# Kernel optimization log

Measured on AMD Instinct MI355X. Metric: run time of the kernel, lower is better.

## Reference

```python
import jax, jax.numpy as jnp
import numpy as np

EMBED_DIM = 1024
NUM_HEADS = 16
HEAD_DIM = EMBED_DIM // NUM_HEADS


def setup_inputs() -> dict:
    key = jax.random.key(0)
    ks = jax.random.split(key, 9)
    B, L, D = 4, 2048, EMBED_DIM
    s = 1.0 / np.sqrt(D)
    return {
        "inputs": jax.random.normal(ks[0], (B, L, D), dtype=jnp.float32),
        "wq": jax.random.normal(ks[1], (D, D), dtype=jnp.float32) * s,
        "bq": jax.random.normal(ks[2], (D,), dtype=jnp.float32) * s,
        "wk": jax.random.normal(ks[3], (D, D), dtype=jnp.float32) * s,
        "bk": jax.random.normal(ks[4], (D,), dtype=jnp.float32) * s,
        "wv": jax.random.normal(ks[5], (D, D), dtype=jnp.float32) * s,
        "bv": jax.random.normal(ks[6], (D,), dtype=jnp.float32) * s,
        "wo": jax.random.normal(ks[7], (D, D), dtype=jnp.float32) * s,
        "bo": jax.random.normal(ks[8], (D,), dtype=jnp.float32) * s,
    }


def reference(inputs, wq, bq, wk, bk, wv, bv, wo, bo):
    B, L, D = inputs.shape
    H, Hd = NUM_HEADS, HEAD_DIM
    # Linear projections (torch Linear: x @ W^T + b)
    q = inputs @ wq.T + bq
    k = inputs @ wk.T + bk
    v = inputs @ wv.T + bv
    # (B, L, D) -> (B, H, L, Hd)
    q = q.reshape(B, L, H, Hd).transpose(0, 2, 1, 3)
    k = k.reshape(B, L, H, Hd).transpose(0, 2, 1, 3)
    v = v.reshape(B, L, H, Hd).transpose(0, 2, 1, 3)
    scale = 1.0 / np.sqrt(Hd).astype(np.float32)
    scores = jnp.einsum("bhqd,bhkd->bhqk", q, k) * scale  # (B,H,L,L)
    attn = jax.nn.softmax(scores, axis=-1)
    out = jnp.einsum("bhqk,bhkd->bhqd", attn, v)  # (B,H,L,Hd)
    out = out.transpose(0, 2, 1, 3).reshape(B, L, D)
    return out @ wo.T + bo
```

## Files before the change

kernel.cpp:

```cpp
#include <hip/hip_runtime.h>

typedef __attribute__((ext_vector_type(8))) short short8;
typedef __attribute__((ext_vector_type(8))) unsigned short ushort8;
typedef __attribute__((ext_vector_type(4))) unsigned short ushort4_t;
typedef __attribute__((ext_vector_type(4))) unsigned u32x4;
typedef __attribute__((ext_vector_type(4))) float f32x4;
typedef __attribute__((ext_vector_type(16))) float f32x16;

#define GLOAD_LDS(gp, lp) \
  __builtin_amdgcn_global_load_lds((const __attribute__((address_space(1))) void*)(gp), \
                                   (__attribute__((address_space(3))) void*)(lp), 16, 0, 0)

static __device__ __forceinline__ unsigned short f2bf(float f) {
  unsigned int u = __float_as_uint(f);
  u = u + 0x7fffu + ((u >> 16) & 1u);
  return (unsigned short)(u >> 16);
}

static __device__ __forceinline__ float exp2i(float x) {
  float r;
  asm("v_exp_f32 %0, %1" : "=v"(r) : "v"(x));
  return r;
}

static __device__ __forceinline__ unsigned cvtpk(float a, float b) {
  unsigned r;
  asm("v_cvt_pk_bf16_f32 %0, %1, %2" : "=v"(r) : "v"(a), "v"(b));
  return r;
}

static __device__ __forceinline__ void pl32swap(unsigned& a, unsigned& b) {
  asm("v_permlane32_swap_b32 %0, %1" : "+v"(a), "+v"(b));
}

__global__ __launch_bounds__(256) void cvt_bf16(const float* __restrict__ in,
                                                unsigned short* __restrict__ out,
                                                int n) {
  int i = (blockIdx.x * 256 + threadIdx.x) * 8;
  if (i >= n) return;
  const float4* p = reinterpret_cast<const float4*>(in + i);
  float4 a = p[0], b = p[1];
  ushort8 o;
  o[0] = f2bf(a.x); o[1] = f2bf(a.y); o[2] = f2bf(a.z); o[3] = f2bf(a.w);
  o[4] = f2bf(b.x); o[5] = f2bf(b.y); o[6] = f2bf(b.z); o[7] = f2bf(b.w);
  *reinterpret_cast<ushort8*>(out + i) = o;
}

__global__ __launch_bounds__(256) void cvt_w4(const float* __restrict__ i0, const float* __restrict__ i1,
                                              const float* __restrict__ i2, const float* __restrict__ i3,
                                              unsigned short* __restrict__ o0, unsigned short* __restrict__ o1,
                                              unsigned short* __restrict__ o2, unsigned short* __restrict__ o3) {
  int w = blockIdx.y;
  const float* in = (w == 0) ? i0 : (w == 1) ? i1 : (w == 2) ? i2 : i3;
  unsigned short* out = (w == 0) ? o0 : (w == 1) ? o1 : (w == 2) ? o2 : o3;
  int i = (blockIdx.x * 256 + threadIdx.x) * 8;
  const float4* p = reinterpret_cast<const float4*>(in + i);
  float4 a = p[0], b = p[1];
  ushort8 o;
  o[0] = f2bf(a.x); o[1] = f2bf(a.y); o[2] = f2bf(a.z); o[3] = f2bf(a.w);
  o[4] = f2bf(b.x); o[5] = f2bf(b.y); o[6] = f2bf(b.z); o[7] = f2bf(b.w);
  *reinterpret_cast<ushort8*>(out + i) = o;
}

template <int MODE>
__global__ __launch_bounds__(256) void gemm_bt(const unsigned short* __restrict__ A,
                                               const unsigned short* __restrict__ B,
                                               const float* __restrict__ bias,
                                               void* __restrict__ Cptr,
                                               int M, int N, int K, float scale) {
  __shared__ char As[2][16384];
  __shared__ char Bs[2][16384];
  const int t = threadIdx.x;
  const int lane = t & 63, wave = t >> 6;
  const int wm = wave >> 1, wn = wave & 1;
  const int m0 = blockIdx.y * 128, n0 = blockIdx.x * 128;

  const unsigned short* aS[4];
  const unsigned short* bS[4];
#pragma unroll
  for (int j = 0; j < 4; j++) {
    int i = wave * 256 + j * 64 + lane;
    int r = i >> 3, c = ((i & 7) ^ (r & 7)) << 3;
    aS[j] = A + (size_t)(m0 + r) * K + c;
    bS[j] = B + (size_t)(n0 + r) * K + c;
  }

  f32x4 acc[4][4] = {};
  const int NT = K >> 6;

#pragma unroll
  for (int j = 0; j < 4; j++) {
    GLOAD_LDS(aS[j], As[0] + wave * 4096 + j * 1024);
    GLOAD_LDS(bS[j], Bs[0] + wave * 4096 + j * 1024);
  }

  for (int kt = 0; kt < NT; kt++) {
    const int cur = kt & 1;
    __syncthreads();
    if (kt + 1 < NT) {
      int ko = (kt + 1) << 6;
#pragma unroll
      for (int j = 0; j < 4; j++) {
        GLOAD_LDS(aS[j] + ko, As[cur ^ 1] + wave * 4096 + j * 1024);
        GLOAD_LDS(bS[j] + ko, Bs[cur ^ 1] + wave * 4096 + j * 1024);
      }
    }
    const char* Ac = As[cur];
    const char* Bc = Bs[cur];
#pragma unroll
    for (int ks = 0; ks < 2; ks++) {
      short8 af[4], bfr[4];
#pragma unroll
      for (int x = 0; x < 4; x++) {
        int arow = wm * 64 + x * 16 + (lane & 15);
        int kk = ks * 32 + (lane >> 4) * 8;
        af[x] = *reinterpret_cast<const short8*>(Ac + (((arow * 64 + kk) * 2) ^ ((arow & 7) << 4)));
        int brow = wn * 64 + x * 16 + (lane & 15);
        bfr[x] = *reinterpret_cast<const short8*>(Bc + (((brow * 64 + kk) * 2) ^ ((brow & 7) << 4)));
      }
      __builtin_amdgcn_s_setprio(1);
#pragma unroll
      for (int mi = 0; mi < 4; mi++)
#pragma unroll
        for (int ni = 0; ni < 4; ni++)
          acc[mi][ni] = __builtin_amdgcn_mfma_f32_16x16x32_bf16(af[mi], bfr[ni], acc[mi][ni], 0, 0, 0);
      __builtin_amdgcn_s_setprio(0);
    }
  }

#pragma unroll
  for (int mi = 0; mi < 4; mi++) {
#pragma unroll
    for (int ni = 0; ni < 4; ni++) {
      int n = n0 + wn * 64 + ni * 16 + (lane & 15);
      float bs = bias[n];
      int mbase = m0 + wm * 64 + mi * 16 + ((lane >> 4) << 2);
      if (MODE == 2) {
        int b = mbase >> 11, l = mbase & 2047;
        ushort4_t o;
#pragma unroll
        for (int r = 0; r < 4; r++) o[r] = f2bf(acc[mi][ni][r] + bs);
        *reinterpret_cast<ushort4_t*>((unsigned short*)Cptr + (size_t)(b * N + n) * 2048 + l) = o;
      } else if (MODE == 0) {
#pragma unroll
        for (int r = 0; r < 4; r++)
          ((unsigned short*)Cptr)[(size_t)(mbase + r) * N + n] = f2bf((acc[mi][ni][r] + bs) * scale);
      } else {
#pragma unroll
        for (int r = 0; r < 4; r++)
          ((float*)Cptr)[(size_t)(mbase + r) * N + n] = acc[mi][ni][r] + bs;
      }
    }
  }
}

__global__ __launch_bounds__(256) void attn_fwd(const unsigned short* __restrict__ Q,
                                                const unsigned short* __restrict__ Kb,
                                                const unsigned short* __restrict__ Vt,
                                                unsigned short* __restrict__ O) {
  const int h = blockIdx.y;
  const int b = blockIdx.z;
  const int q0 = blockIdx.x * 128;
  __shared__ char Ks[2][8192];
  __shared__ char Vs[2][8192];
  const int t = threadIdx.x, lane = t & 63, wave = t >> 6;
  const int ql = lane & 31;
  const int hi = lane >> 5;
  const int qrow = q0 + wave * 32 + ql;
  const int sw = (ql & 7) << 4;

  int lo_[4];
#pragma unroll
  for (int st = 0; st < 4; st++) lo_[st] = (ql * 128 + sw) ^ (st * 32 + hi * 16);

  const int ic0 = wave * 128 + lane, ic1 = ic0 + 64;
  const int r0 = ic0 >> 3, c0 = ((ic0 & 7) ^ (r0 & 7)) << 3;
  const int r1 = ic1 >> 3, c1 = ((ic1 & 7) ^ (r1 & 7)) << 3;
  const unsigned short* kS0 = Kb + (size_t)(b * 2048 + r0) * 1024 + h * 64 + c0;
  const unsigned short* kS1 = Kb + (size_t)(b * 2048 + r1) * 1024 + h * 64 + c1;
  const unsigned short* vS0 = Vt + ((size_t)(b * 16 + h) * 64 + r0) * 2048 + c0;
  const unsigned short* vS1 = Vt + ((size_t)(b * 16 + h) * 64 + r1) * 2048 + c1;

  short8 qf[4];
  {
    const unsigned short* qp = Q + (size_t)(b * 2048 + qrow) * 1024 + h * 64 + hi * 8;
#pragma unroll
    for (int st = 0; st < 4; st++) qf[st] = *reinterpret_cast<const short8*>(qp + st * 16);
  }

  const short one_bf = (short)0x3F80;
  const short8 ones = {one_bf, one_bf, one_bf, one_bf, one_bf, one_bf, one_bf, one_bf};

  f32x16 accd0 = {}, accd1 = {};
  f32x16 accl = {};

  GLOAD_LDS(kS0, Ks[0] + wave * 2048);
  GLOAD_LDS(kS1, Ks[0] + wave * 2048 + 1024);
  GLOAD_LDS(vS0, Vs[0] + wave * 2048);
  GLOAD_LDS(vS1, Vs[0] + wave * 2048 + 1024);

#pragma unroll 2
  for (int kt = 0; kt < 32; kt++) {
    const int cur = kt & 1;
    __syncthreads();
    if (kt + 1 < 32) {
      size_t ko = (size_t)(kt + 1) * 65536;
      int vo = (kt + 1) * 64;
      GLOAD_LDS(kS0 + ko, Ks[cur ^ 1] + wave * 2048);
      GLOAD_LDS(kS1 + ko, Ks[cur ^ 1] + wave * 2048 + 1024);
      GLOAD_LDS(vS0 + vo, Vs[cur ^ 1] + wave * 2048);
      GLOAD_LDS(vS1 + vo, Vs[cur ^ 1] + wave * 2048 + 1024);
    }
    const char* Kc = Ks[cur];
    const char* Vc = Vs[cur];

    f32x16 s0 = {}, s1 = {};
    __builtin_amdgcn_s_setprio(1);
#pragma unroll
    for (int st = 0; st < 4; st++) {
      short8 k0 = *reinterpret_cast<const short8*>(Kc + lo_[st]);
      short8 k1 = *reinterpret_cast<const short8*>(Kc + lo_[st] + 4096);
      s0 = __builtin_amdgcn_mfma_f32_32x32x16_bf16(k0, qf[st], s0, 0, 0, 0);
      s1 = __builtin_amdgcn_mfma_f32_32x32x16_bf16(k1, qf[st], s1, 0, 0, 0);
    }
    __builtin_amdgcn_s_setprio(0);

#pragma unroll
    for (int r = 0; r < 16; r++) s0[r] = exp2i(s0[r]);
#pragma unroll
    for (int r = 0; r < 16; r++) s1[r] = exp2i(s1[r]);

    short8 pf0, pf1, pf2, pf3;
    {
      unsigned w0 = cvtpk(s0[0], s0[1]), w1 = cvtpk(s0[2], s0[3]);
      unsigned w2 = cvtpk(s0[4], s0[5]), w3 = cvtpk(s0[6], s0[7]);
      pl32swap(w0, w2); pl32swap(w1, w3);
      u32x4 p0 = {w0, w1, w2, w3};
      pf0 = __builtin_bit_cast(short8, p0);
      unsigned w4 = cvtpk(s0[8], s0[9]), w5 = cvtpk(s0[10], s0[11]);
      unsigned w6 = cvtpk(s0[12], s0[13]), w7 = cvtpk(s0[14], s0[15]);
      pl32swap(w4, w6); pl32swap(w5, w7);
      u32x4 p1 = {w4, w5, w6, w7};
      pf1 = __builtin_bit_cast(short8, p1);
      unsigned x0 = cvtpk(s1[0], s1[1]), x1 = cvtpk(s1[2], s1[3]);
      unsigned x2 = cvtpk(s1[4], s1[5]), x3 = cvtpk(s1[6], s1[7]);
      pl32swap(x0, x2); pl32swap(x1, x3);
      u32x4 p2 = {x0, x1, x2, x3};
      pf2 = __builtin_bit_cast(short8, p2);
      unsigned x4 = cvtpk(s1[8], s1[9]), x5 = cvtpk(s1[10], s1[11]);
      unsigned x6 = cvtpk(s1[12], s1[13]), x7 = cvtpk(s1[14], s1[15]);
      pl32swap(x4, x6); pl32swap(x5, x7);
      u32x4 p3 = {x4, x5, x6, x7};
      pf3 = __builtin_bit_cast(short8, p3);
    }

    __builtin_amdgcn_s_setprio(1);
#pragma unroll
    for (int st = 0; st < 4; st++) {
      short8 pb = (st == 0) ? pf0 : (st == 1) ? pf1 : (st == 2) ? pf2 : pf3;
      short8 v0 = *reinterpret_cast<const short8*>(Vc + lo_[st]);
      short8 v1 = *reinterpret_cast<const short8*>(Vc + lo_[st] + 4096);
      accd0 = __builtin_amdgcn_mfma_f32_32x32x16_bf16(v0, pb, accd0, 0, 0, 0);
      accd1 = __builtin_amdgcn_mfma_f32_32x32x16_bf16(v1, pb, accd1, 0, 0, 0);
      accl  = __builtin_amdgcn_mfma_f32_32x32x16_bf16(ones, pb, accl, 0, 0, 0);
    }
    __builtin_amdgcn_s_setprio(0);
  }

  float inv = 1.0f / accl[0];
  unsigned short* op = O + (size_t)(b * 2048 + qrow) * 1024 + h * 64;
#pragma unroll
  for (int g = 0; g < 4; g++) {
    ushort4_t o0, o1;
#pragma unroll
    for (int j = 0; j < 4; j++) {
      o0[j] = f2bf(accd0[4 * g + j] * inv);
      o1[j] = f2bf(accd1[4 * g + j] * inv);
    }
    *reinterpret_cast<ushort4_t*>(op + 8 * g + 4 * hi) = o0;
    *reinterpret_cast<ushort4_t*>(op + 32 + 8 * g + 4 * hi) = o1;
  }
}

extern "C" void kernel_launch(void* const* d_in, const int* in_sizes, int n_in,
                              void* d_out, int out_size, void* d_ws, size_t ws_size,
                              hipStream_t stream) {
  const float* X = (const float*)d_in[0];
  const float* wq = (const float*)d_in[1];
  const float* bq = (const float*)d_in[2];
  const float* wk = (const float*)d_in[3];
  const float* bk = (const float*)d_in[4];
  const float* wv = (const float*)d_in[5];
  const float* bv = (const float*)d_in[6];
  const float* wo = (const float*)d_in[7];
  const float* bo = (const float*)d_in[8];

  char* ws = (char*)d_ws;
  const size_t MB = 1024 * 1024;
  unsigned short* Xb  = (unsigned short*)(ws + 0);
  unsigned short* Wqb = (unsigned short*)(ws + 16 * MB);
  unsigned short* Wkb = (unsigned short*)(ws + 18 * MB);
  unsigned short* Wvb = (unsigned short*)(ws + 20 * MB);
  unsigned short* Wob = (unsigned short*)(ws + 22 * MB);
  unsigned short* Qb  = (unsigned short*)(ws + 24 * MB);
  unsigned short* Kb  = (unsigned short*)(ws + 40 * MB);
  unsigned short* Vtb = (unsigned short*)(ws + 56 * MB);
  unsigned short* Ob  = (unsigned short*)(ws + 72 * MB);

  cvt_bf16<<<8388608 / 2048, 256, 0, stream>>>(X, Xb, 8388608);
  cvt_w4<<<dim3(512, 4), 256, 0, stream>>>(wq, wk, wv, wo, Wqb, Wkb, Wvb, Wob);

  const float QSCALE = 0.125f * 1.4426950408889634f;
  dim3 gg(8, 64);
  gemm_bt<0><<<gg, 256, 0, stream>>>(Xb, Wqb, bq, Qb, 8192, 1024, 1024, QSCALE);
  gemm_bt<0><<<gg, 256, 0, stream>>>(Xb, Wkb, bk, Kb, 8192, 1024, 1024, 1.0f);
  gemm_bt<2><<<gg, 256, 0, stream>>>(Xb, Wvb, bv, Vtb, 8192, 1024, 1024, 1.0f);

  attn_fwd<<<dim3(16, 16, 4), 256, 0, stream>>>(Qb, Kb, Vtb, Ob);

  gemm_bt<1><<<gg, 256, 0, stream>>>(Ob, Wob, bo, (float*)d_out, 8192, 1024, 1024, 1.0f);
}
```

Baseline: 213.8 us.

## Merge conversion kernels, fuse QKV GEMMs into one launch, hoist zero accumulator

Merges the input and weight bf16 conversion kernels into a single launch, and fuses the three Q/K/V projection GEMMs into one grid of 24x64 blocks that picks its weight, bias and output layout by block index. The output GEMM gets its own kernel with constant sizes. In attention, the first score MFMA now takes a zero accumulator pinned in registers, so the compiler no longer re-zeroes two 16-wide accumulators every iteration. This cuts launch overhead and gives the GPU more concurrent QKV blocks. The cost is a runtime branch in the GEMM epilogue and more live registers for the zero vector.

```diff
diff --git a/kernel.cpp b/kernel.cpp
--- a/kernel.cpp
+++ b/kernel.cpp
@@ -33,11 +33,25 @@
   asm("v_permlane32_swap_b32 %0, %1" : "+v"(a), "+v"(b));
 }
 
-__global__ __launch_bounds__(256) void cvt_bf16(const float* __restrict__ in,
-                                                unsigned short* __restrict__ out,
-                                                int n) {
-  int i = (blockIdx.x * 256 + threadIdx.x) * 8;
-  if (i >= n) return;
+__global__ __launch_bounds__(256) void cvt_all(const float* __restrict__ X,
+                                               const float* __restrict__ w0, const float* __restrict__ w1,
+                                               const float* __restrict__ w2, const float* __restrict__ w3,
+                                               unsigned short* __restrict__ Xb,
+                                               unsigned short* __restrict__ o0, unsigned short* __restrict__ o1,
+                                               unsigned short* __restrict__ o2, unsigned short* __restrict__ o3) {
+  int bid = blockIdx.x;
+  const float* in;
+  unsigned short* out;
+  int i;
+  if (bid < 4096) {
+    in = X; out = Xb; i = bid * 2048 + threadIdx.x * 8;
+  } else {
+    int idx = bid - 4096;
+    int w = idx >> 9;
+    in = (w == 0) ? w0 : (w == 1) ? w1 : (w == 2) ? w2 : w3;
+    out = (w == 0) ? o0 : (w == 1) ? o1 : (w == 2) ? o2 : o3;
+    i = (idx & 511) * 2048 + threadIdx.x * 8;
+  }
   const float4* p = reinterpret_cast<const float4*>(in + i);
   float4 a = p[0], b = p[1];
   ushort8 o;
@@ -46,34 +60,29 @@
   *reinterpret_cast<ushort8*>(out + i) = o;
 }
 
-__global__ __launch_bounds__(256) void cvt_w4(const float* __restrict__ i0, const float* __restrict__ i1,
-                                              const float* __restrict__ i2, const float* __restrict__ i3,
-                                              unsigned short* __restrict__ o0, unsigned short* __restrict__ o1,
-                                              unsigned short* __restrict__ o2, unsigned short* __restrict__ o3) {
-  int w = blockIdx.y;
-  const float* in = (w == 0) ? i0 : (w == 1) ? i1 : (w == 2) ? i2 : i3;
-  unsigned short* out = (w == 0) ? o0 : (w == 1) ? o1 : (w == 2) ? o2 : o3;
-  int i = (blockIdx.x * 256 + threadIdx.x) * 8;
-  const float4* p = reinterpret_cast<const float4*>(in + i);
-  float4 a = p[0], b = p[1];
-  ushort8 o;
-  o[0] = f2bf(a.x); o[1] = f2bf(a.y); o[2] = f2bf(a.z); o[3] = f2bf(a.w);
-  o[4] = f2bf(b.x); o[5] = f2bf(b.y); o[6] = f2bf(b.z); o[7] = f2bf(b.w);
-  *reinterpret_cast<ushort8*>(out + i) = o;
-}
-
-template <int MODE>
-__global__ __launch_bounds__(256) void gemm_bt(const unsigned short* __restrict__ A,
-                                               const unsigned short* __restrict__ B,
-                                               const float* __restrict__ bias,
-                                               void* __restrict__ Cptr,
-                                               int M, int N, int K, float scale) {
+__global__ __launch_bounds__(256) void gemm_qkv(const unsigned short* __restrict__ A,
+                                                const unsigned short* __restrict__ Wq,
+                                                const unsigned short* __restrict__ Wk,
+                                                const unsigned short* __restrict__ Wv,
+                                                const float* __restrict__ bq,
+                                                const float* __restrict__ bk,
+                                                const float* __restrict__ bv,
+                                                unsigned short* __restrict__ Qb,
+                                                unsigned short* __restrict__ Kb,
+                                                unsigned short* __restrict__ Vtb,
+                                                float qscale) {
+  const int K = 1024, N = 1024;
+  const int which = blockIdx.x >> 3;
+  const unsigned short* B = (which == 0) ? Wq : (which == 1) ? Wk : Wv;
+  const float* bias = (which == 0) ? bq : (which == 1) ? bk : bv;
+  const float scale = (which == 0) ? qscale : 1.0f;
+
   __shared__ char As[2][16384];
   __shared__ char Bs[2][16384];
   const int t = threadIdx.x;
   const int lane = t & 63, wave = t >> 6;
   const int wm = wave >> 1, wn = wave & 1;
-  const int m0 = blockIdx.y * 128, n0 = blockIdx.x * 128;
+  const int m0 = blockIdx.y * 128, n0 = (blockIdx.x & 7) * 128;
 
   const unsigned short* aS[4];
   const unsigned short* bS[4];
@@ -86,7 +95,6 @@
   }
 
   f32x4 acc[4][4] = {};
-  const int NT = K >> 6;
 
 #pragma unroll
   for (int j = 0; j < 4; j++) {
@@ -94,10 +102,10 @@
     GLOAD_LDS(bS[j], Bs[0] + wave * 4096 + j * 1024);
   }
 
-  for (int kt = 0; kt < NT; kt++) {
+  for (int kt = 0; kt < 16; kt++) {
     const int cur = kt & 1;
     __syncthreads();
-    if (kt + 1 < NT) {
+    if (kt + 1 < 16) {
       int ko = (kt + 1) << 6;
 #pragma unroll
       for (int j = 0; j < 4; j++) {
@@ -135,21 +143,96 @@
       int n = n0 + wn * 64 + ni * 16 + (lane & 15);
       float bs = bias[n];
       int mbase = m0 + wm * 64 + mi * 16 + ((lane >> 4) << 2);
-      if (MODE == 2) {
-        int b = mbase >> 11, l = mbase & 2047;
+      if (which == 2) {
+        int bb = mbase >> 11, l = mbase & 2047;
         ushort4_t o;
 #pragma unroll
         for (int r = 0; r < 4; r++) o[r] = f2bf(acc[mi][ni][r] + bs);
-        *reinterpret_cast<ushort4_t*>((unsigned short*)Cptr + (size_t)(b * N + n) * 2048 + l) = o;
-      } else if (MODE == 0) {
+        *reinterpret_cast<ushort4_t*>(Vtb + (size_t)(bb * N + n) * 2048 + l) = o;
+      } else {
+        unsigned short* out = (which == 0) ? Qb : Kb;
 #pragma unroll
         for (int r = 0; r < 4; r++)
-          ((unsigned short*)Cptr)[(size_t)(mbase + r) * N + n] = f2bf((acc[mi][ni][r] + bs) * scale);
-      } else {
-#pragma unroll
-        for (int r = 0; r < 4; r++)
-          ((float*)Cptr)[(size_t)(mbase + r) * N + n] = acc[mi][ni][r] + bs;
+          out[(size_t)(mbase + r) * N + n] = f2bf((acc[mi][ni][r] + bs) * scale);
       }
+    }
+  }
+}
+
+__global__ __launch_bounds__(256) void gemm_out(const unsigned short* __restrict__ A,
+                                                const unsigned short* __restrict__ B,
+                                                const float* __restrict__ bias,
+                                                float* __restrict__ C) {
+  const int K = 1024, N = 1024;
+  __shared__ char As[2][16384];
+  __shared__ char Bs[2][16384];
+  const int t = threadIdx.x;
+  const int lane = t & 63, wave = t >> 6;
+  const int wm = wave >> 1, wn = wave & 1;
+  const int m0 = blockIdx.y * 128, n0 = blockIdx.x * 128;
+
+  const unsigned short* aS[4];
+  const unsigned short* bS[4];
+#pragma unroll
+  for (int j = 0; j < 4; j++) {
+    int i = wave * 256 + j * 64 + lane;
+    int r = i >> 3, c = ((i & 7) ^ (r & 7)) << 3;
+    aS[j] = A + (size_t)(m0 + r) * K + c;
+    bS[j] = B + (size_t)(n0 + r) * K + c;
+  }
+
+  f32x4 acc[4][4] = {};
+
+#pragma unroll
+  for (int j = 0; j < 4; j++) {
+    GLOAD_LDS(aS[j], As[0] + wave * 4096 + j * 1024);
+    GLOAD_LDS(bS[j], Bs[0] + wave * 4096 + j * 1024);
+  }
+
+  for (int kt = 0; kt < 16; kt++) {
+    const int cur = kt & 1;
+    __syncthreads();
+    if (kt + 1 < 16) {
+      int ko = (kt + 1) << 6;
+#pragma unroll
+      for (int j = 0; j < 4; j++) {
+        GLOAD_LDS(aS[j] + ko, As[cur ^ 1] + wave * 4096 + j * 1024);
+        GLOAD_LDS(bS[j] + ko, Bs[cur ^ 1] + wave * 4096 + j * 1024);
+      }
+    }
+    const char* Ac = As[cur];
+    const char* Bc = Bs[cur];
+#pragma unroll
+    for (int ks = 0; ks < 2; ks++) {
+      short8 af[4], bfr[4];
+#pragma unroll
+      for (int x = 0; x < 4; x++) {
+        int arow = wm * 64 + x * 16 + (lane & 15);
+        int kk = ks * 32 + (lane >> 4) * 8;
+        af[x] = *reinterpret_cast<const short8*>(Ac + (((arow * 64 + kk) * 2) ^ ((arow & 7) << 4)));
+        int brow = wn * 64 + x * 16 + (lane & 15);
+        bfr[x] = *reinterpret_cast<const short8*>(Bc + (((brow * 64 + kk) * 2) ^ ((brow & 7) << 4)));
+      }
+      __builtin_amdgcn_s_setprio(1);
+#pragma unroll
+      for (int mi = 0; mi < 4; mi++)
+#pragma unroll
+        for (int ni = 0; ni < 4; ni++)
+          acc[mi][ni] = __builtin_amdgcn_mfma_f32_16x16x32_bf16(af[mi], bfr[ni], acc[mi][ni], 0, 0, 0);
+      __builtin_amdgcn_s_setprio(0);
+    }
+  }
+
+#pragma unroll
+  for (int mi = 0; mi < 4; mi++) {
+#pragma unroll
+    for (int ni = 0; ni < 4; ni++) {
+      int n = n0 + wn * 64 + ni * 16 + (lane & 15);
+      float bs = bias[n];
+      int mbase = m0 + wm * 64 + mi * 16 + ((lane >> 4) << 2);
+#pragma unroll
+      for (int r = 0; r < 4; r++)
+        C[(size_t)(mbase + r) * N + n] = acc[mi][ni][r] + bs;
     }
   }
 }
@@ -188,6 +271,9 @@
     for (int st = 0; st < 4; st++) qf[st] = *reinterpret_cast<const short8*>(qp + st * 16);
   }
 
+  f32x16 Z = {};
+  asm volatile("" : "+v"(Z));
+
   const short one_bf = (short)0x3F80;
   const short8 ones = {one_bf, one_bf, one_bf, one_bf, one_bf, one_bf, one_bf, one_bf};
 
@@ -214,10 +300,16 @@
     const char* Kc = Ks[cur];
     const char* Vc = Vs[cur];
 
-    f32x16 s0 = {}, s1 = {};
+    f32x16 s0, s1;
     __builtin_amdgcn_s_setprio(1);
-#pragma unroll
-    for (int st = 0; st < 4; st++) {
+    {
+      short8 k0 = *reinterpret_cast<const short8*>(Kc + lo_[0]);
+      short8 k1 = *reinterpret_cast<const short8*>(Kc + lo_[0] + 4096);
+      s0 = __builtin_amdgcn_mfma_f32_32x32x16_bf16(k0, qf[0], Z, 0, 0, 0);
+      s1 = __builtin_amdgcn_mfma_f32_32x32x16_bf16(k1, qf[0], Z, 0, 0, 0);
+    }
+#pragma unroll
+    for (int st = 1; st < 4; st++) {
       short8 k0 = *reinterpret_cast<const short8*>(Kc + lo_[st]);
       short8 k1 = *reinterpret_cast<const short8*>(Kc + lo_[st] + 4096);
       s0 = __builtin_amdgcn_mfma_f32_32x32x16_bf16(k0, qf[st], s0, 0, 0, 0);
@@ -307,16 +399,13 @@
   unsigned short* Vtb = (unsigned short*)(ws + 56 * MB);
   unsigned short* Ob  = (unsigned short*)(ws + 72 * MB);
 
-  cvt_bf16<<<8388608 / 2048, 256, 0, stream>>>(X, Xb, 8388608);
-  cvt_w4<<<dim3(512, 4), 256, 0, stream>>>(wq, wk, wv, wo, Wqb, Wkb, Wvb, Wob);
+  cvt_all<<<4096 + 4 * 512, 256, 0, stream>>>(X, wq, wk, wv, wo, Xb, Wqb, Wkb, Wvb, Wob);
 
   const float QSCALE = 0.125f * 1.4426950408889634f;
-  dim3 gg(8, 64);
-  gemm_bt<0><<<gg, 256, 0, stream>>>(Xb, Wqb, bq, Qb, 8192, 1024, 1024, QSCALE);
-  gemm_bt<0><<<gg, 256, 0, stream>>>(Xb, Wkb, bk, Kb, 8192, 1024, 1024, 1.0f);
-  gemm_bt<2><<<gg, 256, 0, stream>>>(Xb, Wvb, bv, Vtb, 8192, 1024, 1024, 1.0f);
+  gemm_qkv<<<dim3(24, 64), 256, 0, stream>>>(Xb, Wqb, Wkb, Wvb, bq, bk, bv,
+                                             Qb, Kb, Vtb, QSCALE);
 
   attn_fwd<<<dim3(16, 16, 4), 256, 0, stream>>>(Qb, Kb, Vtb, Ob);
 
-  gemm_bt<1><<<gg, 256, 0, stream>>>(Ob, Wob, bo, (float*)d_out, 8192, 1024, 1024, 1.0f);
-}
+  gemm_out<<<dim3(8, 64), 256, 0, stream>>>(Ob, Wob, bo, (float*)d_out);
+}
```

Measured after the change: 208.9 us. 2.3% less time.
